# Performance work log

Measured on AMD Instinct MI355X. Metric: run time of the kernel, lower is better.

Reference implementation:

```python
import jax, jax.numpy as jnp
import numpy as np

B, INPUT, N, M, H, OUT = 128, 128, 4096, 128, 512, 128
EPS = 1e-8


def setup_inputs() -> dict:
    key = jax.random.key(0)
    ks = jax.random.split(key, 17)
    rn = lambda i, shape, s=1.0: jax.random.normal(ks[i], shape, dtype=jnp.float32) * s
    sm = lambda x: jax.nn.softmax(x, axis=-1)
    return {
        "inp": rn(0, (B, INPUT)),
        "prev_reads": rn(1, (B, M), 0.01),
        "h_prev": rn(2, (B, H), 0.1),
        "c_prev": rn(3, (B, H), 0.1),
        "prev_read_weights": sm(rn(4, (B, N))),
        "prev_write_weights": sm(rn(5, (B, N))),
        "memory": rn(6, (B, N, M), 0.05),
        "W_ih": rn(7, (4 * H, INPUT + M), 0.02),
        "W_hh": rn(8, (4 * H, H), 0.02),
        "b_ih": jnp.zeros((4 * H,), jnp.float32),
        "b_hh": jnp.zeros((4 * H,), jnp.float32),
        "read_W": rn(9, (H, M + 6), 0.05),
        "read_b": jnp.zeros((M + 6,), jnp.float32),
        "write_W": rn(10, (H, 3 * M + 6), 0.05),
        "write_b": jnp.zeros((3 * M + 6,), jnp.float32),
        "fc_W": rn(11, (H + M, OUT), 0.05),
        "fc_b": rn(12, (OUT,), 0.01),
    }


def _lstm_cell(x, h, c, W_ih, W_hh, b_ih, b_hh):
    gates = x @ W_ih.T + h @ W_hh.T + b_ih + b_hh  # [B,4H]
    i, f, g, o = jnp.split(gates, 4, axis=-1)      # torch LSTMCell gate order
    c_new = jax.nn.sigmoid(f) * c + jax.nn.sigmoid(i) * jnp.tanh(g)
    h_new = jax.nn.sigmoid(o) * jnp.tanh(c_new)
    return h_new, c_new


def _address(memory, prev_w, k, beta, g, s, gamma):
    # content addressing: cosine similarity of key k [B,M] vs memory [B,N,M]
    dot = jnp.einsum("bnm,bm->bn", memory, k)
    norm = jnp.linalg.norm(memory, axis=-1) * jnp.linalg.norm(k, axis=-1, keepdims=True)
    sim = dot / (norm + EPS)
    w_c = jax.nn.softmax(beta[:, None] * sim, axis=-1)          # [B,N]
    w_g = g[:, None] * w_c + (1.0 - g[:, None]) * prev_w        # interpolation
    # circular convolution with 3-tap shift distribution s [B,3] (shifts -1,0,+1)
    w_t = (s[:, 0:1] * jnp.roll(w_g, 1, axis=1)
           + s[:, 1:2] * w_g
           + s[:, 2:3] * jnp.roll(w_g, -1, axis=1))
    # sharpening
    w_sh = (w_t + EPS) ** gamma[:, None]
    return w_sh / jnp.sum(w_sh, axis=-1, keepdims=True)


def _split_addr(p):
    k = jnp.tanh(p[:, :M])
    beta = jax.nn.softplus(p[:, M])
    g = jax.nn.sigmoid(p[:, M + 1])
    s = jax.nn.softmax(p[:, M + 2:M + 5], axis=-1)
    gamma = 1.0 + jax.nn.softplus(p[:, M + 5])
    return k, beta, g, s, gamma


def reference(inp, prev_reads, h_prev, c_prev, prev_read_weights, prev_write_weights,
              memory, W_ih, W_hh, b_ih, b_hh, read_W, read_b, write_W, write_b,
              fc_W, fc_b):
    # controller step on cat([inp] + prev_reads)
    x = jnp.concatenate([inp, prev_reads], axis=1)
    h, c = _lstm_cell(x, h_prev, c_prev, W_ih, W_hh, b_ih, b_hh)

    # read head: address then read (memory before any write, per original loop order)
    rp = h @ read_W + read_b
    read_w = _address(memory, prev_read_weights, *_split_addr(rp))
    read_vec = jnp.einsum("bn,bnm->bm", read_w, memory)

    # write head: address, then erase/add
    wp = h @ write_W + write_b
    write_w = _address(memory, prev_write_weights, *_split_addr(wp[:, :M + 6]))
    e = jax.nn.sigmoid(wp[:, M + 6:2 * M + 6])
    a = jnp.tanh(wp[:, 2 * M + 6:])
    w3 = write_w[:, :, None]
    new_memory = memory * (1.0 - w3 * e[:, None, :]) + w3 * a[:, None, :]

    out = jax.nn.sigmoid(jnp.concatenate([h, read_vec], axis=1) @ fc_W + fc_b)
    return (out, read_vec, h, c, read_w, write_w, new_memory)
```

## Files before the change

kernel.cpp:

```cpp
#include <hip/hip_runtime.h>
#include <math.h>

#define B_ 128
#define INPUT_ 128
#define N_ 4096
#define M_ 128
#define H_ 512
#define OUT_ 128
#define EPS_ 1e-8f

typedef float f4v __attribute__((ext_vector_type(4)));

#define OUT_OFF    0
#define RV_OUT_OFF 16384
#define H_OFF      32768
#define C_OFF      98304
#define RW_OFF     163840
#define WW_OFF     688128
#define NM_OFF     1212416

#define KR_OFF     0
#define KW_OFF     16384
#define E_OFF      32768
#define A_OFF      49152
#define PRR_OFF    65536
#define PRW_OFF    66560
#define SIMR_OFF   67584
#define SIMW_OFF   591872
#define RVACC_OFF  1116160
#define PART_OFF   1132544

#define KSPLIT 8
#define KPER   96
#define BO     64

#define J_FULL 524
#define J_PAD  576
#define KS2    4

__device__ __forceinline__ float sigmoidf_(float x){ return 1.0f/(1.0f+expf(-x)); }
__device__ __forceinline__ float softplusf_(float x){ return fmaxf(x,0.0f) + log1pf(expf(-fabsf(x))); }

__global__ __launch_bounds__(256) void k1a_gemm(
    const float* __restrict__ inp, const float* __restrict__ prev_reads,
    const float* __restrict__ h_prev,
    const float* __restrict__ W_ih, const float* __restrict__ W_hh,
    float* __restrict__ part)
{
  __shared__ float wt[32*68];
  __shared__ float xs[32*128];
  int t = threadIdx.x;
  int O0 = blockIdx.x * BO;
  int ks = blockIdx.y;
  int oq = t >> 5, bq = t & 31;
  float acc[8][4];
  #pragma unroll
  for (int i=0;i<8;++i)
    #pragma unroll
    for (int c=0;c<4;++c) acc[i][c]=0.f;

  for (int st = 0; st < 3; ++st) {
    int kg0 = ks*KPER + st*32;
    __syncthreads();
    {
      int o = t >> 2, kq = t & 3;
      int j = O0 + o;
      const float* wsrc; int col;
      if (kg0 < 256) { wsrc = W_ih + (size_t)j*256; col = kg0; }
      else           { wsrc = W_hh + (size_t)j*512; col = kg0 - 256; }
      float4 a0 = *(const float4*)(wsrc + col + kq*8);
      float4 a1 = *(const float4*)(wsrc + col + kq*8 + 4);
      int kk = kq*8;
      wt[(kk+0)*68+o]=a0.x; wt[(kk+1)*68+o]=a0.y; wt[(kk+2)*68+o]=a0.z; wt[(kk+3)*68+o]=a0.w;
      wt[(kk+4)*68+o]=a1.x; wt[(kk+5)*68+o]=a1.y; wt[(kk+6)*68+o]=a1.z; wt[(kk+7)*68+o]=a1.w;
    }
    {
      int b = t >> 1, kq = t & 1;
      const float* src; int col;
      if (kg0 < 128)      { src = inp        + (size_t)b*128; col = kg0; }
      else if (kg0 < 256) { src = prev_reads + (size_t)b*128; col = kg0-128; }
      else                { src = h_prev     + (size_t)b*512; col = kg0-256; }
      #pragma unroll
      for (int r = 0; r < 4; ++r) {
        float4 v = *(const float4*)(src + col + kq*16 + r*4);
        int kk = kq*16 + r*4;
        xs[(kk+0)*128+b]=v.x; xs[(kk+1)*128+b]=v.y; xs[(kk+2)*128+b]=v.z; xs[(kk+3)*128+b]=v.w;
      }
    }
    __syncthreads();
    #pragma unroll
    for (int kk = 0; kk < 32; ++kk) {
      float4 wa = *(const float4*)&wt[kk*68 + oq*8];
      float4 wb = *(const float4*)&wt[kk*68 + oq*8 + 4];
      float4 xv = *(const float4*)&xs[kk*128 + bq*4];
      float wv[8] = {wa.x,wa.y,wa.z,wa.w,wb.x,wb.y,wb.z,wb.w};
      float xx[4] = {xv.x,xv.y,xv.z,xv.w};
      #pragma unroll
      for (int i=0;i<8;++i)
        #pragma unroll
        for (int c=0;c<4;++c)
          acc[i][c] += wv[i]*xx[c];
    }
  }
  #pragma unroll
  for (int i=0;i<8;++i) {
    int j = O0 + oq*8 + i;
    float4 v = make_float4(acc[i][0],acc[i][1],acc[i][2],acc[i][3]);
    *(float4*)(part + ((size_t)ks*2048 + j)*128 + bq*4) = v;
  }
}

__global__ __launch_bounds__(128) void k1b_act(
    const float* __restrict__ part, const float* __restrict__ c_prev,
    const float* __restrict__ b_ih, const float* __restrict__ b_hh,
    float* __restrict__ h_out, float* __restrict__ c_out)
{
  int u = blockIdx.x;
  int b = threadIdx.x;
  float g[4];
  #pragma unroll
  for (int q=0;q<4;++q) {
    int j = q*H_ + u;
    float s = b_ih[j] + b_hh[j];
    #pragma unroll
    for (int ksp=0;ksp<KSPLIT;++ksp)
      s += part[((size_t)ksp*2048 + j)*128 + b];
    g[q] = s;
  }
  float ig = sigmoidf_(g[0]), fg = sigmoidf_(g[1]);
  float gg = tanhf(g[2]),     og = sigmoidf_(g[3]);
  float cn = fg * c_prev[(size_t)b*H_ + u] + ig*gg;
  float hn = og * tanhf(cn);
  c_out[(size_t)b*H_ + u] = cn;
  h_out[(size_t)b*H_ + u] = hn;
}

__global__ __launch_bounds__(256) void k2a_gemm(
    const float* __restrict__ h,
    const float* __restrict__ read_W, const float* __restrict__ write_W,
    float* __restrict__ part)
{
  __shared__ float wt[32*68];
  __shared__ float xs[32*128];
  int t = threadIdx.x;
  int j0 = blockIdx.x * 64;
  int ks = blockIdx.y;
  int jq = t >> 5, bq = t & 31;
  float acc[8][4];
  #pragma unroll
  for (int i=0;i<8;++i)
    #pragma unroll
    for (int c=0;c<4;++c) acc[i][c]=0.f;

  for (int st = 0; st < 4; ++st) {
    int k0 = ks*128 + st*32;
    __syncthreads();
    for (int e = t; e < 32*64; e += 256) {
      int kk = e >> 6, j = e & 63;
      int jc = j0 + j;
      int u = k0 + kk;
      float v = 0.f;
      if (jc < 134)          v = read_W[(size_t)u*134 + jc];
      else if (jc < J_FULL)  v = write_W[(size_t)u*390 + (jc-134)];
      wt[kk*68 + j] = v;
    }
    {
      int b = t >> 1, kq = t & 1;
      const float* src = h + (size_t)b*512 + k0 + kq*16;
      #pragma unroll
      for (int r = 0; r < 4; ++r) {
        float4 v = *(const float4*)(src + r*4);
        int kk = kq*16 + r*4;
        xs[(kk+0)*128+b]=v.x; xs[(kk+1)*128+b]=v.y; xs[(kk+2)*128+b]=v.z; xs[(kk+3)*128+b]=v.w;
      }
    }
    __syncthreads();
    #pragma unroll
    for (int kk = 0; kk < 32; ++kk) {
      float4 wa = *(const float4*)&wt[kk*68 + jq*8];
      float4 wb = *(const float4*)&wt[kk*68 + jq*8 + 4];
      float4 xv = *(const float4*)&xs[kk*128 + bq*4];
      float wv[8] = {wa.x,wa.y,wa.z,wa.w,wb.x,wb.y,wb.z,wb.w};
      float xx[4] = {xv.x,xv.y,xv.z,xv.w};
      #pragma unroll
      for (int i=0;i<8;++i)
        #pragma unroll
        for (int c=0;c<4;++c)
          acc[i][c] += wv[i]*xx[c];
    }
  }
  #pragma unroll
  for (int c=0;c<4;++c) {
    int b = bq*4 + c;
    float4 v0 = make_float4(acc[0][c],acc[1][c],acc[2][c],acc[3][c]);
    float4 v1 = make_float4(acc[4][c],acc[5][c],acc[6][c],acc[7][c]);
    *(float4*)(part + ((size_t)ks*128 + b)*J_PAD + j0 + jq*8)     = v0;
    *(float4*)(part + ((size_t)ks*128 + b)*J_PAD + j0 + jq*8 + 4) = v1;
  }
}

__global__ __launch_bounds__(256) void k2b_post(
    const float* __restrict__ part,
    const float* __restrict__ read_b, const float* __restrict__ write_b,
    float* __restrict__ ws)
{
  int b = blockIdx.x, t = threadIdx.x;
  __shared__ float raw[J_FULL];
  __shared__ float red[128];
  for (int j = t; j < J_FULL; j += 256) {
    float s = (j < 134) ? read_b[j] : write_b[j-134];
    #pragma unroll
    for (int ks = 0; ks < KS2; ++ks)
      s += part[((size_t)ks*128 + b)*J_PAD + j];
    raw[j] = s;
  }
  __syncthreads();
  float krv = 0.f, kwv = 0.f;
  if (t < 128) {
    krv = tanhf(raw[t]);
    kwv = tanhf(raw[134+t]);
    ws[KR_OFF + b*M_ + t] = krv;
    ws[KW_OFF + b*M_ + t] = kwv;
    ws[E_OFF  + b*M_ + t] = sigmoidf_(raw[268+t]);
    ws[A_OFF  + b*M_ + t] = tanhf(raw[396+t]);
  }
  if (t < 128) red[t] = krv*krv;
  __syncthreads();
  for (int s = 64; s > 0; s >>= 1) { if (t < s) red[t] += red[t+s]; __syncthreads(); }
  float nr = sqrtf(red[0]);
  __syncthreads();
  if (t < 128) red[t] = kwv*kwv;
  __syncthreads();
  for (int s = 64; s > 0; s >>= 1) { if (t < s) red[t] += red[t+s]; __syncthreads(); }
  float nw = sqrtf(red[0]);
  if (t == 0) {
    float beta = softplusf_(raw[128]);
    float g    = sigmoidf_(raw[129]);
    float s0 = raw[130], s1 = raw[131], s2 = raw[132];
    float mx = fmaxf(s0, fmaxf(s1, s2));
    float e0 = expf(s0-mx), e1 = expf(s1-mx), e2 = expf(s2-mx);
    float es = e0+e1+e2;
    float gamma = 1.0f + softplusf_(raw[133]);
    float* pr = ws + PRR_OFF + b*8;
    pr[0]=beta; pr[1]=g; pr[2]=gamma; pr[3]=e0/es; pr[4]=e1/es; pr[5]=e2/es; pr[6]=nr;
  }
  if (t == 1) {
    float beta = softplusf_(raw[262]);
    float g    = sigmoidf_(raw[263]);
    float s0 = raw[264], s1 = raw[265], s2 = raw[266];
    float mx = fmaxf(s0, fmaxf(s1, s2));
    float e0 = expf(s0-mx), e1 = expf(s1-mx), e2 = expf(s2-mx);
    float es = e0+e1+e2;
    float gamma = 1.0f + softplusf_(raw[267]);
    float* pr = ws + PRW_OFF + b*8;
    pr[0]=beta; pr[1]=g; pr[2]=gamma; pr[3]=e0/es; pr[4]=e1/es; pr[5]=e2/es; pr[6]=nw;
  }
}

__global__ __launch_bounds__(256) void k3_sim(const float* __restrict__ memory,
                                              float* __restrict__ ws)
{
  int b = blockIdx.y, t = threadIdx.x;
  int n0 = blockIdx.x * 64;
  __shared__ float skr[128], skw[128];
  if (t < 128) { skr[t] = ws[KR_OFF + b*M_ + t]; skw[t] = ws[KW_OFF + b*M_ + t]; }
  __syncthreads();
  float knr = ws[PRR_OFF + b*8 + 6];
  float knw = ws[PRW_OFF + b*8 + 6];
  int wave = t >> 6, lane = t & 63, half = lane >> 5, l32 = lane & 31;
  int m0 = l32 * 4;
  #pragma unroll
  for (int i = 0; i < 8; ++i) {
    int n = n0 + i*8 + wave*2 + half;
    const float4* row = (const float4*)(memory + ((size_t)b*N_ + n)*M_);
    float4 v = row[l32];
    float dr = v.x*skr[m0] + v.y*skr[m0+1] + v.z*skr[m0+2] + v.w*skr[m0+3];
    float dw = v.x*skw[m0] + v.y*skw[m0+1] + v.z*skw[m0+2] + v.w*skw[m0+3];
    float ss = v.x*v.x + v.y*v.y + v.z*v.z + v.w*v.w;
    #pragma unroll
    for (int msk = 16; msk >= 1; msk >>= 1) {
      dr += __shfl_xor(dr, msk, 64);
      dw += __shfl_xor(dw, msk, 64);
      ss += __shfl_xor(ss, msk, 64);
    }
    if (l32 == 0) {
      float nm = sqrtf(ss);
      ws[SIMR_OFF + (size_t)b*N_ + n] = dr / (nm*knr + EPS_);
      ws[SIMW_OFF + (size_t)b*N_ + n] = dw / (nm*knw + EPS_);
    }
  }
}

__global__ __launch_bounds__(512) void k4_addr(
    const float* __restrict__ prev_rw, const float* __restrict__ prev_ww,
    float* __restrict__ ws, float* __restrict__ d_out)
{
  int which = blockIdx.x, b = blockIdx.y, t = threadIdx.x;
  int wid = t >> 6, lane = t & 63;
  const float* sim  = ws + (which ? SIMW_OFF : SIMR_OFF) + (size_t)b*N_;
  const float* prev = (which ? prev_ww : prev_rw) + (size_t)b*N_;
  const float* pr   = ws + (which ? PRW_OFF : PRR_OFF) + b*8;
  float* outw = d_out + (which ? WW_OFF : RW_OFF) + (size_t)b*N_;
  float beta = pr[0], g = pr[1], gamma = pr[2], s0 = pr[3], s1 = pr[4], s2 = pr[5];

  __shared__ float w[N_];
  __shared__ float redmax[8], redsum[8], redp[8];

  float vv[8];
  float mx = -1e30f;
  #pragma unroll
  for (int k = 0; k < 8; ++k) {
    int i = t + k*512;
    float v = beta * sim[i];
    vv[k] = v;
    mx = fmaxf(mx, v);
  }
  #pragma unroll
  for (int m = 1; m <= 32; m <<= 1) mx = fmaxf(mx, __shfl_xor(mx, m, 64));
  if (lane == 0) redmax[wid] = mx;
  __syncthreads();
  mx = redmax[0];
  #pragma unroll
  for (int j = 1; j < 8; ++j) mx = fmaxf(mx, redmax[j]);

  float sum = 0.f;
  #pragma unroll
  for (int k = 0; k < 8; ++k) {
    float v = __expf(vv[k] - mx);
    vv[k] = v;
    sum += v;
  }
  #pragma unroll
  for (int m = 1; m <= 32; m <<= 1) sum += __shfl_xor(sum, m, 64);
  if (lane == 0) redsum[wid] = sum;
  __syncthreads();
  sum = 0.f;
  #pragma unroll
  for (int j = 0; j < 8; ++j) sum += redsum[j];
  float inv = 1.0f / sum;

  #pragma unroll
  for (int k = 0; k < 8; ++k) {
    int i = t + k*512;
    w[i] = g * vv[k] * inv + (1.0f - g) * prev[i];
  }
  __syncthreads();

  float p[8]; float psum = 0.f;
  #pragma unroll
  for (int k = 0; k < 8; ++k) {
    int i = t + k*512;
    float wt = s0 * w[(i-1)&(N_-1)] + s1 * w[i] + s2 * w[(i+1)&(N_-1)];
    float v = __expf(gamma * __logf(wt + EPS_));
    p[k] = v; psum += v;
  }
  #pragma unroll
  for (int m = 1; m <= 32; m <<= 1) psum += __shfl_xor(psum, m, 64);
  if (lane == 0) redp[wid] = psum;
  __syncthreads();
  psum = 0.f;
  #pragma unroll
  for (int j = 0; j < 8; ++j) psum += redp[j];
  float pinv = 1.0f / psum;
  #pragma unroll
  for (int k = 0; k < 8; ++k) {
    int i = t + k*512;
    outw[i] = p[k] * pinv;
  }
}

__global__ __launch_bounds__(256) void k5_update(
    const float* __restrict__ memory, float* __restrict__ d_out,
    float* __restrict__ ws, float* __restrict__ rvp)
{
  int br = 127 - blockIdx.y;
  int txr = 63 - blockIdx.x;
  int t = threadIdx.x;
  int n0 = txr * 64;
  __shared__ float se[128], sa[128];
  __shared__ float rvsh[8][128];
  if (t < 128) {
    se[t] = ws[E_OFF + br*M_ + t];
    sa[t] = ws[A_OFF + br*M_ + t];
  }
  __syncthreads();
  const float* rw  = d_out + RW_OFF + (size_t)br*N_;
  const float* wwp = d_out + WW_OFF + (size_t)br*N_;
  float* nm = d_out + NM_OFF;
  int wave = t >> 6, lane = t & 63, half = lane >> 5, l32 = lane & 31;
  int slot = wave*2 + half;
  int m0 = l32 * 4;
  float rx = 0.f, ry = 0.f, rz = 0.f, rw4 = 0.f;
  #pragma unroll
  for (int i = 0; i < 8; ++i) {
    int n = n0 + i*8 + slot;
    size_t off = ((size_t)br*N_ + n) * M_;
    float4 v = ((const float4*)(memory + off))[l32];
    float rwn = rw[n], wwn = wwp[n];
    rx += rwn*v.x; ry += rwn*v.y; rz += rwn*v.z; rw4 += rwn*v.w;
    f4v o;
    o.x = v.x * (1.0f - wwn*se[m0+0]) + wwn*sa[m0+0];
    o.y = v.y * (1.0f - wwn*se[m0+1]) + wwn*sa[m0+1];
    o.z = v.z * (1.0f - wwn*se[m0+2]) + wwn*sa[m0+2];
    o.w = v.w * (1.0f - wwn*se[m0+3]) + wwn*sa[m0+3];
    __builtin_nontemporal_store(o, (f4v*)(nm + off) + l32);
  }
  rvsh[slot][m0+0] = rx;
  rvsh[slot][m0+1] = ry;
  rvsh[slot][m0+2] = rz;
  rvsh[slot][m0+3] = rw4;
  __syncthreads();
  if (t < 128) {
    float s = 0.f;
    #pragma unroll
    for (int j = 0; j < 8; ++j) s += rvsh[j][t];
    rvp[((size_t)br*64 + txr)*128 + t] = s;
  }
}

__global__ __launch_bounds__(128) void k6_fc(
    const float* __restrict__ fc_W, const float* __restrict__ fc_b,
    float* __restrict__ d_out, const float* __restrict__ rvp)
{
  int b = blockIdx.x, t = threadIdx.x;
  __shared__ float xh[H_ + M_];
  for (int i = t; i < H_; i += 128) xh[i] = d_out[H_OFF + b*H_ + i];
  float rv = 0.f;
  #pragma unroll 8
  for (int tile = 0; tile < 64; ++tile)
    rv += rvp[((size_t)b*64 + tile)*128 + t];
  xh[H_ + t] = rv;
  d_out[RV_OUT_OFF + b*M_ + t] = rv;
  __syncthreads();
  float acc = fc_b[t];
  for (int j = 0; j < H_ + M_; ++j) acc += xh[j] * fc_W[j*OUT_ + t];
  d_out[OUT_OFF + b*OUT_ + t] = sigmoidf_(acc);
}

extern "C" void kernel_launch(void* const* d_in, const int* in_sizes, int n_in,
                              void* d_out, int out_size, void* d_ws, size_t ws_size,
                              hipStream_t stream)
{
  const float* inp        = (const float*)d_in[0];
  const float* prev_reads = (const float*)d_in[1];
  const float* h_prev     = (const float*)d_in[2];
  const float* c_prev     = (const float*)d_in[3];
  const float* prev_rw    = (const float*)d_in[4];
  const float* prev_ww    = (const float*)d_in[5];
  const float* memory     = (const float*)d_in[6];
  const float* W_ih       = (const float*)d_in[7];
  const float* W_hh       = (const float*)d_in[8];
  const float* b_ih       = (const float*)d_in[9];
  const float* b_hh       = (const float*)d_in[10];
  const float* read_W     = (const float*)d_in[11];
  const float* read_b     = (const float*)d_in[12];
  const float* write_W    = (const float*)d_in[13];
  const float* write_b    = (const float*)d_in[14];
  const float* fc_W       = (const float*)d_in[15];
  const float* fc_b       = (const float*)d_in[16];
  float* out = (float*)d_out;
  float* ws  = (float*)d_ws;

  k1a_gemm<<<dim3(32, KSPLIT), 256, 0, stream>>>(inp, prev_reads, h_prev,
                                                 W_ih, W_hh, ws + PART_OFF);
  k1b_act<<<512, 128, 0, stream>>>(ws + PART_OFF, c_prev, b_ih, b_hh,
                                   out + H_OFF, out + C_OFF);
  k2a_gemm<<<dim3(9, KS2), 256, 0, stream>>>(out + H_OFF, read_W, write_W,
                                             ws + PART_OFF);
  k2b_post<<<B_, 256, 0, stream>>>(ws + PART_OFF, read_b, write_b, ws);
  k3_sim<<<dim3(64, B_), 256, 0, stream>>>(memory, ws);
  k4_addr<<<dim3(2, B_), 512, 0, stream>>>(prev_rw, prev_ww, ws, out);
  k5_update<<<dim3(64, B_), 256, 0, stream>>>(memory, out, ws, ws + PART_OFF);
  k6_fc<<<B_, 128, 0, stream>>>(fc_W, fc_b, out, ws + PART_OFF);
}
```

Baseline: 216.1 us.

## Process memory stages in batch groups for L2/LLC reuse; batch fc over 4 rows

The sim, addressing and update kernels now run in two batch groups of 64, so memory read by k3 is more likely still in the last-level cache when k5 reads it again. The reversed block order in k5, which served the same reuse purpose, is dropped. k6_fc now handles four batch rows per block so each fc_W load is reused four times. The cost is more kernel launches and less parallelism per launch in the k4 and k6 stages.

```diff
diff --git a/kernel.cpp b/kernel.cpp
--- a/kernel.cpp
+++ b/kernel.cpp
@@ -37,6 +37,8 @@
 #define J_FULL 524
 #define J_PAD  576
 #define KS2    4
+
+#define GRP    64
 
 __device__ __forceinline__ float sigmoidf_(float x){ return 1.0f/(1.0f+expf(-x)); }
 __device__ __forceinline__ float softplusf_(float x){ return fmaxf(x,0.0f) + log1pf(expf(-fabsf(x))); }
@@ -258,9 +260,9 @@
 }
 
 __global__ __launch_bounds__(256) void k3_sim(const float* __restrict__ memory,
-                                              float* __restrict__ ws)
-{
-  int b = blockIdx.y, t = threadIdx.x;
+                                              float* __restrict__ ws, int b0)
+{
+  int b = b0 + blockIdx.y, t = threadIdx.x;
   int n0 = blockIdx.x * 64;
   __shared__ float skr[128], skw[128];
   if (t < 128) { skr[t] = ws[KR_OFF + b*M_ + t]; skw[t] = ws[KW_OFF + b*M_ + t]; }
@@ -293,9 +295,9 @@
 
 __global__ __launch_bounds__(512) void k4_addr(
     const float* __restrict__ prev_rw, const float* __restrict__ prev_ww,
-    float* __restrict__ ws, float* __restrict__ d_out)
-{
-  int which = blockIdx.x, b = blockIdx.y, t = threadIdx.x;
+    float* __restrict__ ws, float* __restrict__ d_out, int b0)
+{
+  int which = blockIdx.x, b = b0 + blockIdx.y, t = threadIdx.x;
   int wid = t >> 6, lane = t & 63;
   const float* sim  = ws + (which ? SIMW_OFF : SIMR_OFF) + (size_t)b*N_;
   const float* prev = (which ? prev_ww : prev_rw) + (size_t)b*N_;
@@ -371,21 +373,21 @@
 
 __global__ __launch_bounds__(256) void k5_update(
     const float* __restrict__ memory, float* __restrict__ d_out,
-    float* __restrict__ ws, float* __restrict__ rvp)
-{
-  int br = 127 - blockIdx.y;
-  int txr = 63 - blockIdx.x;
+    float* __restrict__ ws, float* __restrict__ rvp, int b0)
+{
+  int b = b0 + blockIdx.y;
+  int tx = blockIdx.x;
   int t = threadIdx.x;
-  int n0 = txr * 64;
+  int n0 = tx * 64;
   __shared__ float se[128], sa[128];
   __shared__ float rvsh[8][128];
   if (t < 128) {
-    se[t] = ws[E_OFF + br*M_ + t];
-    sa[t] = ws[A_OFF + br*M_ + t];
-  }
-  __syncthreads();
-  const float* rw  = d_out + RW_OFF + (size_t)br*N_;
-  const float* wwp = d_out + WW_OFF + (size_t)br*N_;
+    se[t] = ws[E_OFF + b*M_ + t];
+    sa[t] = ws[A_OFF + b*M_ + t];
+  }
+  __syncthreads();
+  const float* rw  = d_out + RW_OFF + (size_t)b*N_;
+  const float* wwp = d_out + WW_OFF + (size_t)b*N_;
   float* nm = d_out + NM_OFF;
   int wave = t >> 6, lane = t & 63, half = lane >> 5, l32 = lane & 31;
   int slot = wave*2 + half;
@@ -394,7 +396,7 @@
   #pragma unroll
   for (int i = 0; i < 8; ++i) {
     int n = n0 + i*8 + slot;
-    size_t off = ((size_t)br*N_ + n) * M_;
+    size_t off = ((size_t)b*N_ + n) * M_;
     float4 v = ((const float4*)(memory + off))[l32];
     float rwn = rw[n], wwn = wwp[n];
     rx += rwn*v.x; ry += rwn*v.y; rz += rwn*v.z; rw4 += rwn*v.w;
@@ -414,7 +416,7 @@
     float s = 0.f;
     #pragma unroll
     for (int j = 0; j < 8; ++j) s += rvsh[j][t];
-    rvp[((size_t)br*64 + txr)*128 + t] = s;
+    rvp[((size_t)b*64 + tx)*128 + t] = s;
   }
 }
 
@@ -422,19 +424,32 @@
     const float* __restrict__ fc_W, const float* __restrict__ fc_b,
     float* __restrict__ d_out, const float* __restrict__ rvp)
 {
-  int b = blockIdx.x, t = threadIdx.x;
-  __shared__ float xh[H_ + M_];
-  for (int i = t; i < H_; i += 128) xh[i] = d_out[H_OFF + b*H_ + i];
-  float rv = 0.f;
-  #pragma unroll 8
-  for (int tile = 0; tile < 64; ++tile)
-    rv += rvp[((size_t)b*64 + tile)*128 + t];
-  xh[H_ + t] = rv;
-  d_out[RV_OUT_OFF + b*M_ + t] = rv;
-  __syncthreads();
-  float acc = fc_b[t];
-  for (int j = 0; j < H_ + M_; ++j) acc += xh[j] * fc_W[j*OUT_ + t];
-  d_out[OUT_OFF + b*OUT_ + t] = sigmoidf_(acc);
+  int b0 = blockIdx.x * 4, t = threadIdx.x;
+  __shared__ float xh[4][H_ + M_];
+  #pragma unroll
+  for (int q = 0; q < 4; ++q)
+    for (int i = t; i < H_; i += 128)
+      xh[q][i] = d_out[H_OFF + (size_t)(b0+q)*H_ + i];
+  #pragma unroll
+  for (int q = 0; q < 4; ++q) {
+    float rv = 0.f;
+    #pragma unroll 8
+    for (int tile = 0; tile < 64; ++tile)
+      rv += rvp[((size_t)(b0+q)*64 + tile)*128 + t];
+    xh[q][H_ + t] = rv;
+    d_out[RV_OUT_OFF + (size_t)(b0+q)*M_ + t] = rv;
+  }
+  __syncthreads();
+  float bias = fc_b[t];
+  float a0 = bias, a1 = bias, a2 = bias, a3 = bias;
+  for (int j = 0; j < H_ + M_; ++j) {
+    float w = fc_W[(size_t)j*OUT_ + t];
+    a0 += xh[0][j]*w; a1 += xh[1][j]*w; a2 += xh[2][j]*w; a3 += xh[3][j]*w;
+  }
+  d_out[OUT_OFF + (size_t)(b0+0)*OUT_ + t] = sigmoidf_(a0);
+  d_out[OUT_OFF + (size_t)(b0+1)*OUT_ + t] = sigmoidf_(a1);
+  d_out[OUT_OFF + (size_t)(b0+2)*OUT_ + t] = sigmoidf_(a2);
+  d_out[OUT_OFF + (size_t)(b0+3)*OUT_ + t] = sigmoidf_(a3);
 }
 
 extern "C" void kernel_launch(void* const* d_in, const int* in_sizes, int n_in,
@@ -468,8 +483,11 @@
   k2a_gemm<<<dim3(9, KS2), 256, 0, stream>>>(out + H_OFF, read_W, write_W,
                                              ws + PART_OFF);
   k2b_post<<<B_, 256, 0, stream>>>(ws + PART_OFF, read_b, write_b, ws);
-  k3_sim<<<dim3(64, B_), 256, 0, stream>>>(memory, ws);
-  k4_addr<<<dim3(2, B_), 512, 0, stream>>>(prev_rw, prev_ww, ws, out);
-  k5_update<<<dim3(64, B_), 256, 0, stream>>>(memory, out, ws, ws + PART_OFF);
-  k6_fc<<<B_, 128, 0, stream>>>(fc_W, fc_b, out, ws + PART_OFF);
-}
+  for (int g = 0; g < B_ / GRP; ++g) {
+    k3_sim<<<dim3(64, GRP), 256, 0, stream>>>(memory, ws, g*GRP);
+    k4_addr<<<dim3(2, GRP), 512, 0, stream>>>(prev_rw, prev_ww, ws, out, g*GRP);
+    k5_update<<<dim3(64, GRP), 256, 0, stream>>>(memory, out, ws,
+                                                 ws + PART_OFF, g*GRP);
+  }
+  k6_fc<<<B_/4, 128, 0, stream>>>(fc_W, fc_b, out, ws + PART_OFF);
+}
```

Result: slower. 253.9 us (+17.5%).
